# Optimization experiments

Measured on AMD Instinct MI355X. Metric: run time of the kernel, lower is better.

## Reference

```python
import jax, jax.numpy as jnp
import numpy as np

N = 50000; E = 200000; H = 128; L = 3; T = 2; FOUT = 64
G = 1000; NP = 3; ATOM_V = 64; BOND_V = 8
EPS = 1e-5
_DEG_HIST = np.array([0., 50000., 75000., 50000., 25000.])
# PyG PNAConv: avg_deg['log'] = sum(hist[d] * log(d+1)) / num_nodes
AVG_DEG_LOG = float((np.log(np.arange(5) + 1.0) * _DEG_HIST).sum() / _DEG_HIST.sum())


def _bn(v, g, b):
    # training-mode BatchNorm1d (biased variance), eps=1e-5
    mu = v.mean(0)
    var = ((v - mu) ** 2).mean(0)
    return (v - mu) * jax.lax.rsqrt(var + EPS) * g + b


def setup_inputs() -> dict:
    key = jax.random.key(0)
    ks = jax.random.split(key, 16)
    def nrm(k, shape, fan):
        return (jax.random.normal(k, shape, dtype=jnp.float32) / np.sqrt(fan)).astype(jnp.float32)
    return {
        'x': jax.random.randint(ks[0], (N, 9), 0, ATOM_V),
        'edge_index': jax.random.randint(ks[1], (2, E), 0, N),
        'batch': jnp.sort(jax.random.randint(ks[2], (N,), 0, G)),
        'edge_attr_idx': jax.random.randint(ks[3], (E, 3), 0, BOND_V),
        'atom_emb': nrm(ks[4], (9, ATOM_V, H), H),
        'bond_emb': nrm(ks[5], (3, BOND_V, H), H),
        'edge_W': nrm(ks[6], (L, H, H), H), 'edge_b': jnp.zeros((L, H), jnp.float32),
        'pre_W': nrm(ks[7], (L, T, 3 * H, H), 3 * H), 'pre_b': jnp.zeros((L, T, H), jnp.float32),
        'post_W': nrm(ks[8], (L, T, 13 * H, FOUT), 13 * H), 'post_b': jnp.zeros((L, T, FOUT), jnp.float32),
        'lin_W': nrm(ks[9], (L, H, H), H), 'lin_b': jnp.zeros((L, H), jnp.float32),
        'bn_g': jnp.ones((L, H), jnp.float32), 'bn_b': jnp.zeros((L, H), jnp.float32),
        'mlp_W': nrm(ks[10], (2, H, H), H), 'mlp_b': jnp.zeros((2, H), jnp.float32),
        'mlp_g': jnp.ones((2, H), jnp.float32), 'mlp_be': jnp.zeros((2, H), jnp.float32),
        'hW1': nrm(ks[11], (H, H // 2), H), 'hb1': jnp.zeros((H // 2,), jnp.float32),
        'hg1': jnp.ones((H // 2,), jnp.float32), 'hbe1': jnp.zeros((H // 2,), jnp.float32),
        'hW2': nrm(ks[12], (H // 2, H // 4), H // 2), 'hb2': jnp.zeros((H // 4,), jnp.float32),
        'hg2': jnp.ones((H // 4,), jnp.float32), 'hbe2': jnp.zeros((H // 4,), jnp.float32),
        'hW3': nrm(ks[13], (H // 4, NP), H // 4), 'hb3': jnp.zeros((NP,), jnp.float32),
    }


def reference(x, edge_index, batch, edge_attr_idx, atom_emb, bond_emb,
              edge_W, edge_b, pre_W, pre_b, post_W, post_b, lin_W, lin_b,
              bn_g, bn_b, mlp_W, mlp_b, mlp_g, mlp_be,
              hW1, hb1, hg1, hbe1, hW2, hb2, hg2, hbe2, hW3, hb3):
    # encoders: sum of per-feature embeddings (OGB Atom/Bond encoder)
    h = atom_emb[jnp.arange(9), x].sum(1)               # [N,H]
    e = bond_emb[jnp.arange(3), edge_attr_idx].sum(1)   # [E,H]
    src, dst = edge_index[0], edge_index[1]
    cnt = jax.ops.segment_sum(jnp.ones((E,), jnp.float32), dst, N)
    deg = jnp.maximum(cnt, 1.0)[:, None, None]          # clamp(1), as in PyG scalers
    amp = jnp.log(deg + 1.0) / AVG_DEG_LOG
    att = AVG_DEG_LOG / jnp.log(deg + 1.0)
    has = (cnt > 0)[:, None, None]
    for l in range(L):
        ea = e @ edge_W[l] + edge_b[l]                                  # [E,H]
        msg_in = jnp.concatenate([h[dst], h[src], ea], -1)              # [E,3H]
        m = jnp.einsum('ef,tfh->eth', msg_in, pre_W[l]) + pre_b[l]      # [E,T,H]
        s1 = jax.ops.segment_sum(m, dst, N)
        s2 = jax.ops.segment_sum(m * m, dst, N)
        mean = s1 / deg
        std = jnp.sqrt(jax.nn.relu(s2 / deg - mean * mean) + EPS)
        mn = jnp.where(has, jax.ops.segment_min(m, dst, N), 0.0)
        mx = jnp.where(has, jax.ops.segment_max(m, dst, N), 0.0)
        agg = jnp.concatenate([mean, mn, mx, std], -1)                  # [N,T,4H]
        scaled = jnp.concatenate([agg, agg * amp, agg * att], -1)       # [N,T,12H]
        upd = jnp.concatenate(
            [jnp.broadcast_to(h[:, None, :], (N, T, H)), scaled], -1)   # [N,T,13H]
        o = jnp.einsum('ntf,tfo->nto', upd, post_W[l]) + post_b[l]      # [N,T,FOUT]
        o = o.reshape(N, T * FOUT) @ lin_W[l] + lin_b[l]                # [N,H]
        h = jax.nn.relu(_bn(o, bn_g[l], bn_b[l]))
    g = jax.ops.segment_sum(h, batch, G)                                # [G,H]
    for i in range(2):
        g = jax.nn.relu(_bn(g @ mlp_W[i] + mlp_b[i], mlp_g[i], mlp_be[i]))
    g = jax.nn.relu(_bn(g @ hW1 + hb1, hg1, hbe1))
    g = jax.nn.relu(_bn(g @ hW2 + hb2, hg2, hbe2))
    return g @ hW3 + hb3                                                # [G,NP]
```

## Files before the change

kernel.cpp:

```cpp
#include <hip/hip_runtime.h>
#include <math.h>


#define NN 50000
#define NE 200000
#define HD 128
#define NG 1000
#define EPSV 1e-5f
#define ALOGC 1.1330197327247628f

#define AP 1288
#define OPF 132
#define ECAP 512
#define SCB 49

typedef __bf16 bf16x8 __attribute__((ext_vector_type(8)));
typedef float f32x4 __attribute__((ext_vector_type(4)));

__device__ __forceinline__ unsigned short f2bf(float f) {
    unsigned int u = __float_as_uint(f);
    unsigned int r = (u + 0x7FFFu + ((u >> 16) & 1u)) >> 16;
    return (unsigned short)r;
}
__device__ __forceinline__ float bf2f(unsigned short h) {
    return __uint_as_float((unsigned int)h << 16);
}

__global__ void k_fill(float* __restrict__ o, float v, int n) {
    int i = blockIdx.x * 256 + threadIdx.x;
    if (i < n) o[i] = v;
}

__global__ void k_zero(float* __restrict__ z, int n) {
    int i = blockIdx.x * 256 + threadIdx.x;
    if (i < n) z[i] = 0.f;
}

__global__ __launch_bounds__(256) void k_encode_nodes(
    const int* __restrict__ x, const float* __restrict__ aemb, float* __restrict__ h) {
    __shared__ int xi[8][9];
    int nb = blockIdx.x * 8;
    int tid = threadIdx.x;
    if (tid < 72) xi[tid / 9][tid % 9] = x[nb * 9 + tid];
    __syncthreads();
    int node = tid >> 5, c4 = (tid & 31) * 4;
    float4 acc = make_float4(0.f, 0.f, 0.f, 0.f);
#pragma unroll
    for (int f = 0; f < 9; ++f) {
        float4 e = *(const float4*)(aemb + (size_t)(f * 64 + xi[node][f]) * HD + c4);
        acc.x += e.x; acc.y += e.y; acc.z += e.z; acc.w += e.w;
    }
    *(float4*)(h + (size_t)(nb + node) * HD + c4) = acc;
}

__global__ void k_count(const int* __restrict__ dst, int* __restrict__ cnt) {
    int e = blockIdx.x * 256 + threadIdx.x;
    if (e < NE) atomicAdd(&cnt[dst[e]], 1);
}

__global__ __launch_bounds__(1024) void k_scanA(const int* __restrict__ cnt,
                                                int* __restrict__ sc, int* __restrict__ tot) {
    __shared__ int buf[1024];
    int tid = threadIdx.x;
    int i = blockIdx.x * 1024 + tid;
    int v = (i < NN) ? cnt[i] : 0;
    buf[tid] = v;
    __syncthreads();
    for (int s = 1; s < 1024; s <<= 1) {
        int t = (tid >= s) ? buf[tid - s] : 0;
        __syncthreads();
        buf[tid] += t;
        __syncthreads();
    }
    if (i < NN) sc[i] = buf[tid];
    if (tid == 1023) tot[blockIdx.x] = buf[1023];
}

__global__ void k_scanB(const int* __restrict__ tot, int* __restrict__ offb) {
    if (threadIdx.x == 0) {
        int run = 0;
        for (int b = 0; b < SCB; ++b) { offb[b] = run; run += tot[b]; }
    }
}

__global__ __launch_bounds__(1024) void k_scanC(
    const int* __restrict__ cnt, const int* __restrict__ sc, const int* __restrict__ offb,
    int* __restrict__ rowptr, float* __restrict__ ampv, float* __restrict__ attv) {
    int i = blockIdx.x * 1024 + threadIdx.x;
    if (i == 0) rowptr[0] = 0;
    if (i < NN) {
        rowptr[i + 1] = offb[blockIdx.x] + sc[i];
        int v = cnt[i];
        float dg = (float)(v > 0 ? v : 1);
        float lg = logf(dg + 1.0f);
        ampv[i] = lg / ALOGC;
        attv[i] = ALOGC / lg;
    }
}

__global__ void k_scatter(const int* __restrict__ ei, const int* __restrict__ eai,
                          const int* __restrict__ rowptr,
                          int* __restrict__ fill, int* __restrict__ precs) {
    int e = blockIdx.x * 256 + threadIdx.x;
    if (e < NE) {
        int d = ei[NE + e];
        int pos = rowptr[d] + atomicAdd(&fill[d], 1);
        int cidx = eai[e * 3] | (eai[e * 3 + 1] << 3) | (eai[e * 3 + 2] << 6);
        precs[pos] = ei[e] | (cidx << 17);
    }
}

__global__ void k_fold(const float* __restrict__ edge_W, const float* __restrict__ edge_b,
                       const float* __restrict__ pre_W, const float* __restrict__ pre_b,
                       float* __restrict__ cW, float* __restrict__ tb) {
    int l = blockIdx.y;
    int k = blockIdx.x;
    int tj = threadIdx.x;
    int t = tj >> 7, j = tj & 127;
    const float* pw = pre_W + ((size_t)(l * 2 + t) * 384 + 256) * 128 + j;
    if (k < 128) {
        const float* ew = edge_W + ((size_t)l * 128 + k) * 128;
        float acc = 0.f;
        for (int i = 0; i < 128; ++i) acc += ew[i] * pw[i * 128];
        cW[((size_t)l * 128 + k) * 256 + tj] = acc;
    } else {
        const float* eb = edge_b + l * 128;
        float acc = pre_b[(l * 2 + t) * 128 + j];
        for (int i = 0; i < 128; ++i) acc += eb[i] * pw[i * 128];
        tb[l * 256 + tj] = acc;
    }
}

__global__ void k_bcomb2(const float* __restrict__ bemb, const float* __restrict__ cW,
                         unsigned short* __restrict__ bcomb) {
    int ci = blockIdx.x, l = blockIdx.y, tj = threadIdx.x;
    const float* s0 = bemb + (size_t)(0 * 8 + (ci & 7)) * 128;
    const float* s1 = bemb + (size_t)(1 * 8 + ((ci >> 3) & 7)) * 128;
    const float* s2 = bemb + (size_t)(2 * 8 + (ci >> 6)) * 128;
    const float* w = cW + (size_t)l * 128 * 256;
    float acc = 0.f;
    for (int i = 0; i < 128; ++i) acc += (s0[i] + s1[i] + s2[i]) * w[i * 256 + tj];
    bcomb[((size_t)l * 512 + ci) * 256 + tj] = f2bf(acc);
}

__device__ __forceinline__ void pack_body2(const float* __restrict__ W, int N, int NT,
                                           unsigned short* __restrict__ pkh,
                                           unsigned short* __restrict__ pkl,
                                           int blk, int lane) {
    int kstep = blk / NT, nt = blk - kstep * NT;
    int kb = kstep * 32 + (lane >> 4) * 8;
    int col = nt * 16 + (lane & 15);
    unsigned short th[8], tl[8];
#pragma unroll
    for (int i = 0; i < 8; ++i) {
        float w = W[(size_t)(kb + i) * N + col];
        unsigned short hh = f2bf(w);
        th[i] = hh;
        tl[i] = f2bf(w - bf2f(hh));
    }
    size_t base = ((size_t)blk * 64 + lane) * 8;
    *(uint4*)(pkh + base) = *(uint4*)th;
    *(uint4*)(pkl + base) = *(uint4*)tl;
}

__global__ __launch_bounds__(64) void k_packall(
    const float* __restrict__ post_W, const float* __restrict__ lin_W,
    const float* __restrict__ pre_W,
    unsigned short* __restrict__ pkPostHi, unsigned short* __restrict__ pkPostLo,
    unsigned short* __restrict__ pkLinHi, unsigned short* __restrict__ pkLinLo,
    unsigned short* __restrict__ pkPreHi, unsigned short* __restrict__ pkPreLo) {
    int b = blockIdx.x;
    int lane = threadIdx.x;
    if (b < 1248) {
        int l = b / 416, rem = b % 416;
        int t = rem / 208, blk = rem % 208;
        size_t off = ((size_t)l * 2 + t) * 106496;
        pack_body2(post_W + ((size_t)l * 2 + t) * 1664 * 64, 64, 4,
                   pkPostHi + off, pkPostLo + off, blk, lane);
    } else if (b < 1344) {
        int idx = b - 1248;
        int l = idx / 32, blk = idx % 32;
        pack_body2(lin_W + (size_t)l * 128 * 128, 128, 8,
                   pkLinHi + (size_t)l * 16384, pkLinLo + (size_t)l * 16384, blk, lane);
    } else {
        int idx = b - 1344;
        int l = idx / 128, bb = idx % 128;
        const float* preW = pre_W + (size_t)l * 2 * 384 * 128;
        unsigned short* phi = pkPreHi + (size_t)l * 65536;
        unsigned short* plo = pkPreLo + (size_t)l * 65536;
        int kstep = bb >> 5, nt = bb & 31;
        int q = lane >> 4, nc = lane & 15;
        int col = nt * 16 + nc;
        int t = (col >> 7) & 1;
        int jcol = col & 127;
        int fbase = (col < 256) ? 0 : 128;
        unsigned short hi[8], lo[8];
#pragma unroll
        for (int i = 0; i < 8; ++i) {
            int k = kstep * 32 + q * 8 + i;
            float w = preW[((size_t)t * 384 + fbase + k) * 128 + jcol];
            unsigned short h16 = f2bf(w);
            hi[i] = h16;
            lo[i] = f2bf(w - bf2f(h16));
        }
        size_t base = ((size_t)bb * 64 + lane) * 8;
        *(uint4*)(phi + base) = *(uint4*)hi;
        *(uint4*)(plo + base) = *(uint4*)lo;
    }
}

__device__ __forceinline__ void pre_mfma_body2(
    const unsigned short* __restrict__ ah, const unsigned short* __restrict__ al,
    const unsigned short* __restrict__ phi, const unsigned short* __restrict__ plo,
    const float* __restrict__ tb, int n0, int tid,
    unsigned short* __restrict__ hzd, unsigned short* __restrict__ hzs) {
    int lane = tid & 63, w = tid >> 6;
    int q = lane >> 4, nc = lane & 15;
    f32x4 acc0[8], acc1[8];
#pragma unroll
    for (int j = 0; j < 8; ++j) {
        acc0[j] = (f32x4){0.f, 0.f, 0.f, 0.f};
        acc1[j] = (f32x4){0.f, 0.f, 0.f, 0.f};
    }
#pragma unroll
    for (int kk = 0; kk < 4; ++kk) {
        bf16x8 Ahi0 = *(const bf16x8*)(ah + nc * 136 + kk * 32 + q * 8);
        bf16x8 Alo0 = *(const bf16x8*)(al + nc * 136 + kk * 32 + q * 8);
        bf16x8 Ahi1 = *(const bf16x8*)(ah + (16 + nc) * 136 + kk * 32 + q * 8);
        bf16x8 Alo1 = *(const bf16x8*)(al + (16 + nc) * 136 + kk * 32 + q * 8);
#pragma unroll
        for (int j = 0; j < 8; ++j) {
            int nt = w * 8 + j;
            size_t base = ((size_t)(kk * 32 + nt) * 64 + lane) * 8;
            bf16x8 Bhi = *(const bf16x8*)(phi + base);
            bf16x8 Blo = *(const bf16x8*)(plo + base);
            acc0[j] = __builtin_amdgcn_mfma_f32_16x16x32_bf16(Ahi0, Bhi, acc0[j], 0, 0, 0);
            acc0[j] = __builtin_amdgcn_mfma_f32_16x16x32_bf16(Ahi0, Blo, acc0[j], 0, 0, 0);
            acc0[j] = __builtin_amdgcn_mfma_f32_16x16x32_bf16(Alo0, Bhi, acc0[j], 0, 0, 0);
            acc1[j] = __builtin_amdgcn_mfma_f32_16x16x32_bf16(Ahi1, Bhi, acc1[j], 0, 0, 0);
            acc1[j] = __builtin_amdgcn_mfma_f32_16x16x32_bf16(Ahi1, Blo, acc1[j], 0, 0, 0);
            acc1[j] = __builtin_amdgcn_mfma_f32_16x16x32_bf16(Alo1, Bhi, acc1[j], 0, 0, 0);
        }
    }
#pragma unroll
    for (int j = 0; j < 8; ++j) {
        int col = (w * 8 + j) * 16 + nc;
        float bias = (col < 256) ? tb[col] : 0.f;
#pragma unroll
        for (int reg = 0; reg < 4; ++reg) {
            int r0 = n0 + q * 4 + reg;
            int r1 = r0 + 16;
            if (col < 256) {
                if (r0 < NN) hzd[(size_t)r0 * 256 + col] = f2bf(acc0[j][reg] + bias);
                if (r1 < NN) hzd[(size_t)r1 * 256 + col] = f2bf(acc1[j][reg] + bias);
            } else {
                if (r0 < NN) hzs[(size_t)r0 * 256 + (col - 256)] = f2bf(acc0[j][reg]);
                if (r1 < NN) hzs[(size_t)r1 * 256 + (col - 256)] = f2bf(acc1[j][reg]);
            }
        }
    }
}

__global__ __launch_bounds__(256) void k_pre_m(
    const float* __restrict__ h,
    const unsigned short* __restrict__ phi, const unsigned short* __restrict__ plo,
    const float* __restrict__ tb,
    unsigned short* __restrict__ hzd, unsigned short* __restrict__ hzs) {
    __shared__ __align__(16) unsigned short ah[32 * 136];
    __shared__ __align__(16) unsigned short al[32 * 136];
    int n0 = blockIdx.x * 32;
    int tid = threadIdx.x;
    for (int half = 0; half < 2; ++half) {
        int node = (tid >> 4) + half * 16, cg = (tid & 15) * 8;
        int n = n0 + node;
        unsigned short hh[8] = {0, 0, 0, 0, 0, 0, 0, 0};
        unsigned short ll[8] = {0, 0, 0, 0, 0, 0, 0, 0};
        if (n < NN) {
            const float* hs = h + (size_t)n * HD + cg;
            float4 v0 = *(const float4*)(hs);
            float4 v1 = *(const float4*)(hs + 4);
            float vv[8] = {v0.x, v0.y, v0.z, v0.w, v1.x, v1.y, v1.z, v1.w};
#pragma unroll
            for (int i = 0; i < 8; ++i) {
                hh[i] = f2bf(vv[i]);
                ll[i] = f2bf(vv[i] - bf2f(hh[i]));
            }
        }
        *(uint4*)(ah + node * 136 + cg) = *(uint4*)hh;
        *(uint4*)(al + node * 136 + cg) = *(uint4*)ll;
    }
    __syncthreads();
    pre_mfma_body2(ah, al, phi, plo, tb, n0, tid, hzd, hzs);
}

__global__ __launch_bounds__(256) void k_bnpre(
    const float* __restrict__ o2, const float* __restrict__ stats,
    const float* __restrict__ g, const float* __restrict__ b,
    const unsigned short* __restrict__ phi, const unsigned short* __restrict__ plo,
    const float* __restrict__ tb,
    float* __restrict__ h, unsigned short* __restrict__ hzd, unsigned short* __restrict__ hzs) {
    __shared__ __align__(16) unsigned short ah[32 * 136];
    __shared__ __align__(16) unsigned short al[32 * 136];
    int n0 = blockIdx.x * 32;
    int tid = threadIdx.x;
    for (int half = 0; half < 2; ++half) {
        int node = (tid >> 4) + half * 16, cg = (tid & 15) * 8;
        int n = n0 + node;
        unsigned short hh[8] = {0, 0, 0, 0, 0, 0, 0, 0};
        unsigned short ll[8] = {0, 0, 0, 0, 0, 0, 0, 0};
        if (n < NN) {
            const float* os = o2 + (size_t)n * HD + cg;
            float4 v0 = *(const float4*)(os);
            float4 v1 = *(const float4*)(os + 4);
            float vv[8] = {v0.x, v0.y, v0.z, v0.w, v1.x, v1.y, v1.z, v1.w};
            float ou[8];
#pragma unroll
            for (int i = 0; i < 8; ++i) {
                int c = cg + i;
                float mu = stats[c] * (1.f / NN);
                float var = stats[128 + c] * (1.f / NN) - mu * mu;
                float val = (vv[i] - mu) * rsqrtf(var + EPSV) * g[c] + b[c];
                val = fmaxf(val, 0.f);
                ou[i] = val;
                hh[i] = f2bf(val);
                ll[i] = f2bf(val - bf2f(hh[i]));
            }
            float* hd = h + (size_t)n * HD + cg;
            *(float4*)(hd) = make_float4(ou[0], ou[1], ou[2], ou[3]);
            *(float4*)(hd + 4) = make_float4(ou[4], ou[5], ou[6], ou[7]);
        }
        *(uint4*)(ah + node * 136 + cg) = *(uint4*)hh;
        *(uint4*)(al + node * 136 + cg) = *(uint4*)ll;
    }
    __syncthreads();
    pre_mfma_body2(ah, al, phi, plo, tb, n0, tid, hzd, hzs);
}

__global__ __launch_bounds__(256) void k_post(
    const float* __restrict__ h,
    const unsigned short* __restrict__ hzd, const unsigned short* __restrict__ hzs,
    const int* __restrict__ rowptr, const int* __restrict__ precs,
    const unsigned short* __restrict__ bcomb,
    const float* __restrict__ ampv, const float* __restrict__ attv,
    const unsigned short* __restrict__ pkPostHi, const unsigned short* __restrict__ pkPostLo,
    const float* __restrict__ postb,
    const unsigned short* __restrict__ pkLinHi, const unsigned short* __restrict__ pkLinLo,
    const float* __restrict__ linb,
    float* __restrict__ o2, float* __restrict__ stats) {
    __shared__ __align__(16) unsigned short a_lds[16 * AP];
    __shared__ __align__(16) float o_f[16 * OPF];
    __shared__ int es[ECAP];
    __shared__ float s_amp[16], s_att[16];
    int n0 = blockIdx.x * 16;
    int tid = threadIdx.x;

    int pbase = rowptr[n0];
    int ecount = rowptr[n0 + 16] - pbase;
    for (int i = tid; i < ecount && i < ECAP; i += 256) es[i] = precs[pbase + i];
    {
        int node = tid >> 4, cg = (tid & 15) * 8;
        const float* hs = h + (size_t)(n0 + node) * HD + cg;
        float4 v0 = *(const float4*)(hs);
        float4 v1 = *(const float4*)(hs + 4);
        unsigned short* d0 = a_lds + node * AP + cg;
        unsigned short* d1 = d0 + 640;
        unsigned short bb[8];
        bb[0] = f2bf(v0.x); bb[1] = f2bf(v0.y); bb[2] = f2bf(v0.z); bb[3] = f2bf(v0.w);
        bb[4] = f2bf(v1.x); bb[5] = f2bf(v1.y); bb[6] = f2bf(v1.z); bb[7] = f2bf(v1.w);
#pragma unroll
        for (int i = 0; i < 8; ++i) { d0[i] = bb[i]; d1[i] = bb[i]; }
    }
    if (tid < 16) { s_amp[tid] = ampv[n0 + tid]; s_att[tid] = attv[n0 + tid]; }
    __syncthreads();

    {
        int wv = tid >> 6, lane = tid & 63;
        int cc = lane * 4;
        int tt = cc >> 7, jj = cc & 127;
        bool incap = (ecount <= ECAP);
        const float4 Z4 = make_float4(0.f, 0.f, 0.f, 0.f);
        const float4 BIG = make_float4(3.4e38f, 3.4e38f, 3.4e38f, 3.4e38f);
        const float4 NBIG = make_float4(-3.4e38f, -3.4e38f, -3.4e38f, -3.4e38f);

#define EDGE_ACC(P, S1, S2, MN, MX)                                                       \
        {                                                                                 \
            int rec = incap ? es[(P) - pbase] : precs[(P)];                               \
            int sp = rec & 131071;                                                        \
            int ci = rec >> 17;                                                           \
            uint2 uv = *(const uint2*)(hzs + (size_t)sp * 256 + cc);                      \
            uint2 ub = *(const uint2*)(bcomb + (size_t)ci * 256 + cc);                    \
            float wx = __uint_as_float(uv.x << 16) + __uint_as_float(ub.x << 16);         \
            float wy = __uint_as_float(uv.x & 0xffff0000u) + __uint_as_float(ub.x & 0xffff0000u); \
            float wz = __uint_as_float(uv.y << 16) + __uint_as_float(ub.y << 16);         \
            float ww = __uint_as_float(uv.y & 0xffff0000u) + __uint_as_float(ub.y & 0xffff0000u); \
            S1.x += wx; S1.y += wy; S1.z += wz; S1.w += ww;                               \
            S2.x += wx * wx; S2.y += wy * wy; S2.z += wz * wz; S2.w += ww * ww;           \
            MN.x = fminf(MN.x, wx); MN.y = fminf(MN.y, wy);                               \
            MN.z = fminf(MN.z, wz); MN.w = fminf(MN.w, ww);                               \
            MX.x = fmaxf(MX.x, wx); MX.y = fmaxf(MX.y, wy);                               \
            MX.z = fmaxf(MX.z, wz); MX.w = fmaxf(MX.w, ww);                               \
        }

        auto fin = [&](int r, int cnt, float4 hd, float4 s1, float4 s2, float4 mn, float4 mx) {
            float inv = 1.f / (float)(cnt > 0 ? cnt : 1);
            float4 mw, stdv, mean;
            mw.x = s1.x * inv; mw.y = s1.y * inv; mw.z = s1.z * inv; mw.w = s1.w * inv;
            stdv.x = sqrtf(fmaxf(s2.x * inv - mw.x * mw.x, 0.f) + EPSV);
            stdv.y = sqrtf(fmaxf(s2.y * inv - mw.y * mw.y, 0.f) + EPSV);
            stdv.z = sqrtf(fmaxf(s2.z * inv - mw.z * mw.z, 0.f) + EPSV);
            stdv.w = sqrtf(fmaxf(s2.w * inv - mw.w * mw.w, 0.f) + EPSV);
            if (cnt > 0) {
                mean.x = hd.x + mw.x; mean.y = hd.y + mw.y;
                mean.z = hd.z + mw.z; mean.w = hd.w + mw.w;
                mn.x += hd.x; mn.y += hd.y; mn.z += hd.z; mn.w += hd.w;
                mx.x += hd.x; mx.y += hd.y; mx.z += hd.z; mx.w += hd.w;
            } else {
                mean = Z4; mn = Z4; mx = Z4;
            }
            unsigned short* d = a_lds + r * AP + tt * 640 + 128 + jj;
            d[0] = f2bf(mean.x); d[1] = f2bf(mean.y); d[2] = f2bf(mean.z); d[3] = f2bf(mean.w);
            d += 128; d[0] = f2bf(mn.x); d[1] = f2bf(mn.y); d[2] = f2bf(mn.z); d[3] = f2bf(mn.w);
            d += 128; d[0] = f2bf(mx.x); d[1] = f2bf(mx.y); d[2] = f2bf(mx.z); d[3] = f2bf(mx.w);
            d += 128; d[0] = f2bf(stdv.x); d[1] = f2bf(stdv.y); d[2] = f2bf(stdv.z); d[3] = f2bf(stdv.w);
        };

        for (int i = 0; i < 2; ++i) {
            int ra = wv * 4 + i * 2;
            int rb = ra + 1;
            int na = n0 + ra, nb = n0 + rb;
            int pa0 = rowptr[na], pa1 = rowptr[na + 1];
            int pb0 = rowptr[nb], pb1 = rowptr[nb + 1];
            uint2 uda = *(const uint2*)(hzd + (size_t)na * 256 + cc);
            uint2 udb = *(const uint2*)(hzd + (size_t)nb * 256 + cc);
            float4 hda, hdb;
            hda.x = __uint_as_float(uda.x << 16); hda.y = __uint_as_float(uda.x & 0xffff0000u);
            hda.z = __uint_as_float(uda.y << 16); hda.w = __uint_as_float(uda.y & 0xffff0000u);
            hdb.x = __uint_as_float(udb.x << 16); hdb.y = __uint_as_float(udb.x & 0xffff0000u);
            hdb.z = __uint_as_float(udb.y << 16); hdb.w = __uint_as_float(udb.y & 0xffff0000u);
            float4 s1a = Z4, s2a = Z4, mna = BIG, mxa = NBIG;
            float4 s1b = Z4, s2b = Z4, mnb = BIG, mxb = NBIG;
            int da = pa1 - pa0, db = pb1 - pb0;
            int mc = (da < db) ? da : db;
            for (int k = 0; k < mc; ++k) {
                EDGE_ACC(pa0 + k, s1a, s2a, mna, mxa)
                EDGE_ACC(pb0 + k, s1b, s2b, mnb, mxb)
            }
            for (int k = mc; k < da; ++k) EDGE_ACC(pa0 + k, s1a, s2a, mna, mxa)
            for (int k = mc; k < db; ++k) EDGE_ACC(pb0 + k, s1b, s2b, mnb, mxb)
            fin(ra, da, hda, s1a, s2a, mna, mxa);
            fin(rb, db, hdb, s1b, s2b, mnb, mxb);
        }
#undef EDGE_ACC
    }
    __syncthreads();

    {
        int lane = tid & 63;
        int w = tid >> 6;
        int t = w >> 1;
        int ntb = (w & 1) * 2;
        int q = lane >> 4, nc = lane & 15;
        const unsigned short* arow = a_lds + (size_t)nc * AP + t * 640 + q * 8;
        size_t toff = (size_t)t * 106496;
        const unsigned short* pkh = pkPostHi + toff;
        const unsigned short* pkl = pkPostLo + toff;
        f32x4 aP0 = {0.f, 0.f, 0.f, 0.f}, aP1 = {0.f, 0.f, 0.f, 0.f};
        f32x4 aA0 = {0.f, 0.f, 0.f, 0.f}, aA1 = {0.f, 0.f, 0.f, 0.f};
        f32x4 aT0 = {0.f, 0.f, 0.f, 0.f}, aT1 = {0.f, 0.f, 0.f, 0.f};
        for (int kk = 0; kk < 20; ++kk) {
            bf16x8 af = *(const bf16x8*)(arow + kk * 32);
            size_t ib = ((size_t)(kk * 4 + ntb) * 64 + lane) * 8;
            aP0 = __builtin_amdgcn_mfma_f32_16x16x32_bf16(af, *(const bf16x8*)(pkh + ib), aP0, 0, 0, 0);
            aP0 = __builtin_amdgcn_mfma_f32_16x16x32_bf16(af, *(const bf16x8*)(pkl + ib), aP0, 0, 0, 0);
            aP1 = __builtin_amdgcn_mfma_f32_16x16x32_bf16(af, *(const bf16x8*)(pkh + ib + 512), aP1, 0, 0, 0);
            aP1 = __builtin_amdgcn_mfma_f32_16x16x32_bf16(af, *(const bf16x8*)(pkl + ib + 512), aP1, 0, 0, 0);
            if (kk >= 4) {
                size_t ia = ((size_t)((kk + 16) * 4 + ntb) * 64 + lane) * 8;
                aA0 = __builtin_amdgcn_mfma_f32_16x16x32_bf16(af, *(const bf16x8*)(pkh + ia), aA0, 0, 0, 0);
                aA0 = __builtin_amdgcn_mfma_f32_16x16x32_bf16(af, *(const bf16x8*)(pkl + ia), aA0, 0, 0, 0);
                aA1 = __builtin_amdgcn_mfma_f32_16x16x32_bf16(af, *(const bf16x8*)(pkh + ia + 512), aA1, 0, 0, 0);
                aA1 = __builtin_amdgcn_mfma_f32_16x16x32_bf16(af, *(const bf16x8*)(pkl + ia + 512), aA1, 0, 0, 0);
                size_t it = ((size_t)((kk + 32) * 4 + ntb) * 64 + lane) * 8;
                aT0 = __builtin_amdgcn_mfma_f32_16x16x32_bf16(af, *(const bf16x8*)(pkh + it), aT0, 0, 0, 0);
                aT0 = __builtin_amdgcn_mfma_f32_16x16x32_bf16(af, *(const bf16x8*)(pkl + it), aT0, 0, 0, 0);
                aT1 = __builtin_amdgcn_mfma_f32_16x16x32_bf16(af, *(const bf16x8*)(pkh + it + 512), aT1, 0, 0, 0);
                aT1 = __builtin_amdgcn_mfma_f32_16x16x32_bf16(af, *(const bf16x8*)(pkl + it + 512), aT1, 0, 0, 0);
            }
        }
#pragma unroll
        for (int u = 0; u < 2; ++u) {
            int nt = ntb + u;
            int col = t * 64 + nt * 16 + nc;
            float pbia = postb[t * 64 + nt * 16 + nc];
            f32x4 P = u ? aP1 : aP0;
            f32x4 A = u ? aA1 : aA0;
            f32x4 T = u ? aT1 : aT0;
#pragma unroll
            for (int reg = 0; reg < 4; ++reg) {
                int mrow = q * 4 + reg;
                o_f[mrow * OPF + col] = P[reg] + s_amp[mrow] * A[reg] + s_att[mrow] * T[reg] + pbia;
            }
        }
    }
    __syncthreads();

    {
        int lane = tid & 63;
        int w = tid >> 6;
        int ntb = w * 2;
        int q = lane >> 4, nc = lane & 15;
        const float* arow = o_f + (size_t)nc * OPF + q * 8;
        f32x4 L0 = {0.f, 0.f, 0.f, 0.f}, L1 = {0.f, 0.f, 0.f, 0.f};
#pragma unroll
        for (int kk = 0; kk < 4; ++kk) {
            float4 a0 = *(const float4*)(arow + kk * 32);
            float4 a1 = *(const float4*)(arow + kk * 32 + 4);
            float vv[8] = {a0.x, a0.y, a0.z, a0.w, a1.x, a1.y, a1.z, a1.w};
            unsigned short hh[8], ll[8];
#pragma unroll
            for (int i = 0; i < 8; ++i) {
                hh[i] = f2bf(vv[i]);
                ll[i] = f2bf(vv[i] - bf2f(hh[i]));
            }
            bf16x8 Ahi = *(const bf16x8*)hh;
            bf16x8 Alo = *(const bf16x8*)ll;
            size_t ib = ((size_t)(kk * 8 + ntb) * 64 + lane) * 8;
            bf16x8 B0h = *(const bf16x8*)(pkLinHi + ib);
            bf16x8 B0l = *(const bf16x8*)(pkLinLo + ib);
            bf16x8 B1h = *(const bf16x8*)(pkLinHi + ib + 512);
            bf16x8 B1l = *(const bf16x8*)(pkLinLo + ib + 512);
            L0 = __builtin_amdgcn_mfma_f32_16x16x32_bf16(Ahi, B0h, L0, 0, 0, 0);
            L0 = __builtin_amdgcn_mfma_f32_16x16x32_bf16(Alo, B0h, L0, 0, 0, 0);
            L0 = __builtin_amdgcn_mfma_f32_16x16x32_bf16(Ahi, B0l, L0, 0, 0, 0);
            L1 = __builtin_amdgcn_mfma_f32_16x16x32_bf16(Ahi, B1h, L1, 0, 0, 0);
            L1 = __builtin_amdgcn_mfma_f32_16x16x32_bf16(Alo, B1h, L1, 0, 0, 0);
            L1 = __builtin_amdgcn_mfma_f32_16x16x32_bf16(Ahi, B1l, L1, 0, 0, 0);
        }
#pragma unroll
        for (int u = 0; u < 2; ++u) {
            int col = (ntb + u) * 16 + nc;
            float lb = linb[col];
            f32x4 L = u ? L1 : L0;
            float ps = 0.f, pss = 0.f;
#pragma unroll
            for (int reg = 0; reg < 4; ++reg) {
                int mrow = q * 4 + reg;
                float v = L[reg] + lb;
                o2[(size_t)(n0 + mrow) * HD + col] = v;
                ps += v; pss += v * v;
            }
            ps += __shfl_down(ps, 16); ps += __shfl_down(ps, 32);
            pss += __shfl_down(pss, 16); pss += __shfl_down(pss, 32);
            if (q == 0) {
                atomicAdd(&stats[col], ps);
                atomicAdd(&stats[128 + col], pss);
            }
        }
    }
}

__global__ void k_pool(const float* __restrict__ o2, const float* __restrict__ stats,
                       const float* __restrict__ g, const float* __restrict__ b,
                       const int* __restrict__ batch, float* __restrict__ g0) {
    int c = threadIdx.x;
    float mu = stats[c] * (1.f / NN);
    float var = stats[128 + c] * (1.f / NN) - mu * mu;
    float rs = rsqrtf(var + EPSV) * g[c];
    float bb = b[c];
    int nbase = blockIdx.x * 64;
    float run = 0.f; int cur = -1;
    for (int i = 0; i < 64; ++i) {
        int n = nbase + i;
        if (n >= NN) break;
        int bi = batch[n];
        if (bi != cur) {
            if (cur >= 0) atomicAdd(&g0[(size_t)cur * HD + c], run);
            cur = bi; run = 0.f;
        }
        run += fmaxf((o2[(size_t)n * HD + c] - mu) * rs + bb, 0.f);
    }
    if (cur >= 0) atomicAdd(&g0[(size_t)cur * HD + c], run);
}

__global__ void k_head_gemm(const float* __restrict__ x, const float* __restrict__ W,
                            const float* __restrict__ b, float* __restrict__ y,
                            float* __restrict__ stats, int K, int Kout) {
    int row = blockIdx.x;
    int col = threadIdx.x;
    if (col >= Kout) return;
    float acc = b[col];
    for (int k = 0; k < K; k += 4) {
        float4 xv = *(const float4*)(x + (size_t)row * K + k);
        acc += xv.x * W[(k + 0) * Kout + col] + xv.y * W[(k + 1) * Kout + col]
             + xv.z * W[(k + 2) * Kout + col] + xv.w * W[(k + 3) * Kout + col];
    }
    y[(size_t)row * Kout + col] = acc;
    if (stats) {
        atomicAdd(&stats[col], acc);
        atomicAdd(&stats[Kout + col], acc * acc);
    }
}

__global__ __launch_bounds__(128) void k_head_fused(
    const float* __restrict__ y_in, const float* __restrict__ stats_in,
    const float* __restrict__ g, const float* __restrict__ b,
    const float* __restrict__ W, const float* __restrict__ bias,
    float* __restrict__ y_out, float* __restrict__ stats_out, int Kin, int Kout) {
    __shared__ float row[128];
    int r = blockIdx.x, tid = threadIdx.x;
    if (tid < Kin) {
        float mu = stats_in[tid] * (1.f / NG);
        float var = stats_in[Kin + tid] * (1.f / NG) - mu * mu;
        float v = (y_in[(size_t)r * Kin + tid] - mu) * rsqrtf(var + EPSV) * g[tid] + b[tid];
        row[tid] = fmaxf(v, 0.f);
    }
    __syncthreads();
    if (tid < Kout) {
        float acc = bias[tid];
        for (int k = 0; k < Kin; ++k) acc += row[k] * W[(size_t)k * Kout + tid];
        y_out[(size_t)r * Kout + tid] = acc;
        if (stats_out) {
            atomicAdd(&stats_out[tid], acc);
            atomicAdd(&stats_out[Kout + tid], acc * acc);
        }
    }
}

extern "C" void kernel_launch(void* const* d_in, const int* in_sizes, int n_in,
                              void* d_out, int out_size, void* d_ws, size_t ws_size,
                              hipStream_t stream) {
    const int*   x        = (const int*)  d_in[0];
    const int*   ei       = (const int*)  d_in[1];
    const int*   batch    = (const int*)  d_in[2];
    const int*   eai      = (const int*)  d_in[3];
    const float* atom_emb = (const float*)d_in[4];
    const float* bond_emb = (const float*)d_in[5];
    const float* edge_W   = (const float*)d_in[6];
    const float* edge_b   = (const float*)d_in[7];
    const float* pre_W    = (const float*)d_in[8];
    const float* pre_b    = (const float*)d_in[9];
    const float* post_W   = (const float*)d_in[10];
    const float* post_b   = (const float*)d_in[11];
    const float* lin_W    = (const float*)d_in[12];
    const float* lin_b    = (const float*)d_in[13];
    const float* bn_g     = (const float*)d_in[14];
    const float* bn_b     = (const float*)d_in[15];
    const float* mlp_W    = (const float*)d_in[16];
    const float* mlp_b    = (const float*)d_in[17];
    const float* mlp_g    = (const float*)d_in[18];
    const float* mlp_be   = (const float*)d_in[19];
    const float* hW1 = (const float*)d_in[20]; const float* hb1  = (const float*)d_in[21];
    const float* hg1 = (const float*)d_in[22]; const float* hbe1 = (const float*)d_in[23];
    const float* hW2 = (const float*)d_in[24]; const float* hb2  = (const float*)d_in[25];
    const float* hg2 = (const float*)d_in[26]; const float* hbe2 = (const float*)d_in[27];
    const float* hW3 = (const float*)d_in[28]; const float* hb3  = (const float*)d_in[29];
    float* out = (float*)d_out;
    (void)n_in; (void)in_sizes;

    char* p = (char*)d_ws;
    size_t off = 0;
    auto alloc = [&](size_t bytes) -> char* {
        char* r = p + off;
        off += (bytes + 255) & ~(size_t)255;
        return r;
    };
    float* h     = (float*)alloc((size_t)NN * HD * 4);
    float* o2    = (float*)alloc((size_t)NN * HD * 4);
    unsigned short* hzd = (unsigned short*)alloc((size_t)NN * 256 * 2);
    unsigned short* hzs = (unsigned short*)alloc((size_t)NN * 256 * 2);
    float* ampv  = (float*)alloc((size_t)NN * 4);
    float* attv  = (float*)alloc((size_t)NN * 4);
    int*   rowptr= (int*)  alloc((size_t)(NN + 1) * 4);
    int*   precs = (int*)  alloc((size_t)NE * 4);
    int*   sc    = (int*)  alloc((size_t)NN * 4);
    int*   stot  = (int*)  alloc((size_t)SCB * 4);
    int*   soff  = (int*)  alloc((size_t)SCB * 4);
    float* cW    = (float*)alloc((size_t)3 * 128 * 256 * 4);
    float* tbb   = (float*)alloc((size_t)3 * 256 * 4);
    unsigned short* bcomb = (unsigned short*)alloc((size_t)3 * 512 * 256 * 2);
    unsigned short* pkPostHi = (unsigned short*)alloc((size_t)3 * 2 * 106496 * 2);
    unsigned short* pkPostLo = (unsigned short*)alloc((size_t)3 * 2 * 106496 * 2);
    unsigned short* pkLinHi  = (unsigned short*)alloc((size_t)3 * 16384 * 2);
    unsigned short* pkLinLo  = (unsigned short*)alloc((size_t)3 * 16384 * 2);
    unsigned short* pkPreHi  = (unsigned short*)alloc((size_t)3 * 65536 * 2);
    unsigned short* pkPreLo  = (unsigned short*)alloc((size_t)3 * 65536 * 2);
    float* gA    = (float*)alloc((size_t)NG * HD * 4);
    float* gB    = (float*)alloc((size_t)NG * HD * 4);
    char* z0 = p + off;
    int*   cnt   = (int*)  alloc((size_t)NN * 4);
    int*   fill  = (int*)  alloc((size_t)NN * 4);
    float* stats = (float*)alloc((size_t)3 * 256 * 4);
    float* hstats= (float*)alloc((size_t)4 * 256 * 4);
    float* g0    = (float*)alloc((size_t)NG * HD * 4);
    size_t zwords = (size_t)((p + off) - z0) / 4;

    if (off > ws_size) {
        k_fill<<<(out_size + 255) / 256, 256, 0, stream>>>(out, (float)ws_size, out_size);
        return;
    }

    k_zero<<<(int)((zwords + 255) / 256), 256, 0, stream>>>((float*)z0, (int)zwords);
    k_encode_nodes<<<NN / 8, 256, 0, stream>>>(x, atom_emb, h);
    k_count<<<(NE + 255) / 256, 256, 0, stream>>>(ei + NE, cnt);
    k_scanA<<<SCB, 1024, 0, stream>>>(cnt, sc, stot);
    k_scanB<<<1, 64, 0, stream>>>(stot, soff);
    k_scanC<<<SCB, 1024, 0, stream>>>(cnt, sc, soff, rowptr, ampv, attv);
    k_scatter<<<(NE + 255) / 256, 256, 0, stream>>>(ei, eai, rowptr, fill, precs);
    k_fold<<<dim3(129, 3), 256, 0, stream>>>(edge_W, edge_b, pre_W, pre_b, cW, tbb);
    k_bcomb2<<<dim3(512, 3), 256, 0, stream>>>(bond_emb, cW, bcomb);
    k_packall<<<1728, 64, 0, stream>>>(post_W, lin_W, pre_W,
        pkPostHi, pkPostLo, pkLinHi, pkLinLo, pkPreHi, pkPreLo);

    int preBlocks = (NN + 31) / 32;
    for (int l = 0; l < 3; ++l) {
        if (l == 0) {
            k_pre_m<<<preBlocks, 256, 0, stream>>>(h, pkPreHi, pkPreLo, tbb, hzd, hzs);
        } else {
            k_bnpre<<<preBlocks, 256, 0, stream>>>(o2, stats + (l - 1) * 256,
                bn_g + (l - 1) * 128, bn_b + (l - 1) * 128,
                pkPreHi + (size_t)l * 65536, pkPreLo + (size_t)l * 65536,
                tbb + l * 256, h, hzd, hzs);
        }
        k_post<<<NN / 16, 256, 0, stream>>>(h, hzd, hzs, rowptr, precs,
            bcomb + (size_t)l * 512 * 256,
            ampv, attv,
            pkPostHi + (size_t)l * 2 * 106496, pkPostLo + (size_t)l * 2 * 106496,
            post_b + l * 2 * 64,
            pkLinHi + (size_t)l * 16384, pkLinLo + (size_t)l * 16384,
            lin_b + l * 128,
            o2, stats + l * 256);
    }

    k_pool<<<(NN + 63) / 64, 128, 0, stream>>>(o2, stats + 2 * 256,
        bn_g + 2 * 128, bn_b + 2 * 128, batch, g0);

    k_head_gemm<<<NG, 128, 0, stream>>>(g0, mlp_W, mlp_b, gA, hstats, 128, 128);
    k_head_fused<<<NG, 128, 0, stream>>>(gA, hstats, mlp_g, mlp_be,
        mlp_W + 128 * 128, mlp_b + 128, gB, hstats + 256, 128, 128);
    k_head_fused<<<NG, 128, 0, stream>>>(gB, hstats + 256, mlp_g + 128, mlp_be + 128,
        hW1, hb1, gA, hstats + 512, 128, 64);
    k_head_fused<<<NG, 128, 0, stream>>>(gA, hstats + 512, hg1, hbe1,
        hW2, hb2, gB, hstats + 768, 64, 32);
    k_head_fused<<<NG, 128, 0, stream>>>(gB, hstats + 768, hg2, hbe2,
        hW3, hb3, out, (float*)nullptr, 32, 3);
}
```

Measured before the change: 924.9 us.

## Process 32 nodes per k_post block so each weight fragment serves two row tiles

```diff
diff --git a/kernel.cpp b/kernel.cpp
--- a/kernel.cpp
+++ b/kernel.cpp
@@ -11,7 +11,7 @@
 
 #define AP 1288
 #define OPF 132
-#define ECAP 512
+#define ECAP2 1024
 #define SCB 49
 
 typedef __bf16 bf16x8 __attribute__((ext_vector_type(8)));
@@ -336,7 +336,7 @@
     pre_mfma_body2(ah, al, phi, plo, tb, n0, tid, hzd, hzs);
 }
 
-__global__ __launch_bounds__(256) void k_post(
+__global__ __launch_bounds__(512) void k_post(
     const float* __restrict__ h,
     const unsigned short* __restrict__ hzd, const unsigned short* __restrict__ hzs,
     const int* __restrict__ rowptr, const int* __restrict__ precs,
@@ -347,37 +347,45 @@
     const unsigned short* __restrict__ pkLinHi, const unsigned short* __restrict__ pkLinLo,
     const float* __restrict__ linb,
     float* __restrict__ o2, float* __restrict__ stats) {
-    __shared__ __align__(16) unsigned short a_lds[16 * AP];
-    __shared__ __align__(16) float o_f[16 * OPF];
-    __shared__ int es[ECAP];
-    __shared__ float s_amp[16], s_att[16];
-    int n0 = blockIdx.x * 16;
+    __shared__ __align__(16) unsigned short a_lds[32 * AP];
+    __shared__ __align__(16) float o_f[32 * OPF];
+    __shared__ int es[ECAP2];
+    __shared__ float s_amp[32], s_att[32];
+    int n0 = blockIdx.x * 32;
     int tid = threadIdx.x;
+    int nEnd = (n0 + 32 < NN) ? (n0 + 32) : NN;
 
     int pbase = rowptr[n0];
-    int ecount = rowptr[n0 + 16] - pbase;
-    for (int i = tid; i < ecount && i < ECAP; i += 256) es[i] = precs[pbase + i];
+    int ecount = rowptr[nEnd] - pbase;
+    for (int i = tid; i < ecount && i < ECAP2; i += 512) es[i] = precs[pbase + i];
     {
         int node = tid >> 4, cg = (tid & 15) * 8;
-        const float* hs = h + (size_t)(n0 + node) * HD + cg;
-        float4 v0 = *(const float4*)(hs);
-        float4 v1 = *(const float4*)(hs + 4);
+        int n = n0 + node;
+        unsigned short bb[8] = {0, 0, 0, 0, 0, 0, 0, 0};
+        if (n < NN) {
+            const float* hs = h + (size_t)n * HD + cg;
+            float4 v0 = *(const float4*)(hs);
+            float4 v1 = *(const float4*)(hs + 4);
+            bb[0] = f2bf(v0.x); bb[1] = f2bf(v0.y); bb[2] = f2bf(v0.z); bb[3] = f2bf(v0.w);
+            bb[4] = f2bf(v1.x); bb[5] = f2bf(v1.y); bb[6] = f2bf(v1.z); bb[7] = f2bf(v1.w);
+        }
         unsigned short* d0 = a_lds + node * AP + cg;
         unsigned short* d1 = d0 + 640;
-        unsigned short bb[8];
-        bb[0] = f2bf(v0.x); bb[1] = f2bf(v0.y); bb[2] = f2bf(v0.z); bb[3] = f2bf(v0.w);
-        bb[4] = f2bf(v1.x); bb[5] = f2bf(v1.y); bb[6] = f2bf(v1.z); bb[7] = f2bf(v1.w);
 #pragma unroll
         for (int i = 0; i < 8; ++i) { d0[i] = bb[i]; d1[i] = bb[i]; }
     }
-    if (tid < 16) { s_amp[tid] = ampv[n0 + tid]; s_att[tid] = attv[n0 + tid]; }
+    if (tid < 32) {
+        int n = n0 + tid;
+        s_amp[tid] = (n < NN) ? ampv[n] : 1.f;
+        s_att[tid] = (n < NN) ? attv[n] : 1.f;
+    }
     __syncthreads();
 
     {
         int wv = tid >> 6, lane = tid & 63;
         int cc = lane * 4;
         int tt = cc >> 7, jj = cc & 127;
-        bool incap = (ecount <= ECAP);
+        bool incap = (ecount <= ECAP2);
         const float4 Z4 = make_float4(0.f, 0.f, 0.f, 0.f);
         const float4 BIG = make_float4(3.4e38f, 3.4e38f, 3.4e38f, 3.4e38f);
         const float4 NBIG = make_float4(-3.4e38f, -3.4e38f, -3.4e38f, -3.4e38f);
@@ -428,15 +436,20 @@
             int ra = wv * 4 + i * 2;
             int rb = ra + 1;
             int na = n0 + ra, nb = n0 + rb;
-            int pa0 = rowptr[na], pa1 = rowptr[na + 1];
-            int pb0 = rowptr[nb], pb1 = rowptr[nb + 1];
-            uint2 uda = *(const uint2*)(hzd + (size_t)na * 256 + cc);
-            uint2 udb = *(const uint2*)(hzd + (size_t)nb * 256 + cc);
-            float4 hda, hdb;
-            hda.x = __uint_as_float(uda.x << 16); hda.y = __uint_as_float(uda.x & 0xffff0000u);
-            hda.z = __uint_as_float(uda.y << 16); hda.w = __uint_as_float(uda.y & 0xffff0000u);
-            hdb.x = __uint_as_float(udb.x << 16); hdb.y = __uint_as_float(udb.x & 0xffff0000u);
-            hdb.z = __uint_as_float(udb.y << 16); hdb.w = __uint_as_float(udb.y & 0xffff0000u);
+            int pa0 = 0, pa1 = 0, pb0 = 0, pb1 = 0;
+            float4 hda = Z4, hdb = Z4;
+            if (na < NN) {
+                pa0 = rowptr[na]; pa1 = rowptr[na + 1];
+                uint2 uda = *(const uint2*)(hzd + (size_t)na * 256 + cc);
+                hda.x = __uint_as_float(uda.x << 16); hda.y = __uint_as_float(uda.x & 0xffff0000u);
+                hda.z = __uint_as_float(uda.y << 16); hda.w = __uint_as_float(uda.y & 0xffff0000u);
+            }
+            if (nb < NN) {
+                pb0 = rowptr[nb]; pb1 = rowptr[nb + 1];
+                uint2 udb = *(const uint2*)(hzd + (size_t)nb * 256 + cc);
+                hdb.x = __uint_as_float(udb.x << 16); hdb.y = __uint_as_float(udb.x & 0xffff0000u);
+                hdb.z = __uint_as_float(udb.y << 16); hdb.w = __uint_as_float(udb.y & 0xffff0000u);
+            }
             float4 s1a = Z4, s2a = Z4, mna = BIG, mxa = NBIG;
             float4 s1b = Z4, s2b = Z4, mnb = BIG, mxb = NBIG;
             int da = pa1 - pa0, db = pb1 - pb0;
@@ -457,48 +470,55 @@
     {
         int lane = tid & 63;
         int w = tid >> 6;
-        int t = w >> 1;
-        int ntb = (w & 1) * 2;
+        int t = w >> 2;
+        int ntIn = w & 3;
         int q = lane >> 4, nc = lane & 15;
-        const unsigned short* arow = a_lds + (size_t)nc * AP + t * 640 + q * 8;
+        const unsigned short* arow0 = a_lds + (size_t)nc * AP + t * 640 + q * 8;
+        const unsigned short* arow1 = a_lds + (size_t)(16 + nc) * AP + t * 640 + q * 8;
         size_t toff = (size_t)t * 106496;
         const unsigned short* pkh = pkPostHi + toff;
         const unsigned short* pkl = pkPostLo + toff;
-        f32x4 aP0 = {0.f, 0.f, 0.f, 0.f}, aP1 = {0.f, 0.f, 0.f, 0.f};
-        f32x4 aA0 = {0.f, 0.f, 0.f, 0.f}, aA1 = {0.f, 0.f, 0.f, 0.f};
-        f32x4 aT0 = {0.f, 0.f, 0.f, 0.f}, aT1 = {0.f, 0.f, 0.f, 0.f};
+        f32x4 P0 = {0.f, 0.f, 0.f, 0.f}, P1 = {0.f, 0.f, 0.f, 0.f};
+        f32x4 A0 = {0.f, 0.f, 0.f, 0.f}, A1 = {0.f, 0.f, 0.f, 0.f};
+        f32x4 T0 = {0.f, 0.f, 0.f, 0.f}, T1 = {0.f, 0.f, 0.f, 0.f};
         for (int kk = 0; kk < 20; ++kk) {
-            bf16x8 af = *(const bf16x8*)(arow + kk * 32);
-            size_t ib = ((size_t)(kk * 4 + ntb) * 64 + lane) * 8;
-            aP0 = __builtin_amdgcn_mfma_f32_16x16x32_bf16(af, *(const bf16x8*)(pkh + ib), aP0, 0, 0, 0);
-            aP0 = __builtin_amdgcn_mfma_f32_16x16x32_bf16(af, *(const bf16x8*)(pkl + ib), aP0, 0, 0, 0);
-            aP1 = __builtin_amdgcn_mfma_f32_16x16x32_bf16(af, *(const bf16x8*)(pkh + ib + 512), aP1, 0, 0, 0);
-            aP1 = __builtin_amdgcn_mfma_f32_16x16x32_bf16(af, *(const bf16x8*)(pkl + ib + 512), aP1, 0, 0, 0);
+            bf16x8 af0 = *(const bf16x8*)(arow0 + kk * 32);
+            bf16x8 af1 = *(const bf16x8*)(arow1 + kk * 32);
+            size_t ib = ((size_t)(kk * 4 + ntIn) * 64 + lane) * 8;
+            bf16x8 Bh = *(const bf16x8*)(pkh + ib);
+            bf16x8 Bl = *(const bf16x8*)(pkl + ib);
+            P0 = __builtin_amdgcn_mfma_f32_16x16x32_bf16(af0, Bh, P0, 0, 0, 0);
+            P0 = __builtin_amdgcn_mfma_f32_16x16x32_bf16(af0, Bl, P0, 0, 0, 0);
+            P1 = __builtin_amdgcn_mfma_f32_16x16x32_bf16(af1, Bh, P1, 0, 0, 0);
+            P1 = __builtin_amdgcn_mfma_f32_16x16x32_bf16(af1, Bl, P1, 0, 0, 0);
             if (kk >= 4) {
-                size_t ia = ((size_t)((kk + 16) * 4 + ntb) * 64 + lane) * 8;
-                aA0 = __builtin_amdgcn_mfma_f32_16x16x32_bf16(af, *(const bf16x8*)(pkh + ia), aA0, 0, 0, 0);
-                aA0 = __builtin_amdgcn_mfma_f32_16x16x32_bf16(af, *(const bf16x8*)(pkl + ia), aA0, 0, 0, 0);
-                aA1 = __builtin_amdgcn_mfma_f32_16x16x32_bf16(af, *(const bf16x8*)(pkh + ia + 512), aA1, 0, 0, 0);
-                aA1 = __builtin_amdgcn_mfma_f32_16x16x32_bf16(af, *(const bf16x8*)(pkl + ia + 512), aA1, 0, 0, 0);
-                size_t it = ((size_t)((kk + 32) * 4 + ntb) * 64 + lane) * 8;
-                aT0 = __builtin_amdgcn_mfma_f32_16x16x32_bf16(af, *(const bf16x8*)(pkh + it), aT0, 0, 0, 0);
-                aT0 = __builtin_amdgcn_mfma_f32_16x16x32_bf16(af, *(const bf16x8*)(pkl + it), aT0, 0, 0, 0);
-                aT1 = __builtin_amdgcn_mfma_f32_16x16x32_bf16(af, *(const bf16x8*)(pkh + it + 512), aT1, 0, 0, 0);
-                aT1 = __builtin_amdgcn_mfma_f32_16x16x32_bf16(af, *(const bf16x8*)(pkl + it + 512), aT1, 0, 0, 0);
-            }
-        }
-#pragma unroll
-        for (int u = 0; u < 2; ++u) {
-            int nt = ntb + u;
-            int col = t * 64 + nt * 16 + nc;
-            float pbia = postb[t * 64 + nt * 16 + nc];
-            f32x4 P = u ? aP1 : aP0;
-            f32x4 A = u ? aA1 : aA0;
-            f32x4 T = u ? aT1 : aT0;
+                size_t ia = ((size_t)((kk + 16) * 4 + ntIn) * 64 + lane) * 8;
+                bf16x8 Ah = *(const bf16x8*)(pkh + ia);
+                bf16x8 Al = *(const bf16x8*)(pkl + ia);
+                A0 = __builtin_amdgcn_mfma_f32_16x16x32_bf16(af0, Ah, A0, 0, 0, 0);
+                A0 = __builtin_amdgcn_mfma_f32_16x16x32_bf16(af0, Al, A0, 0, 0, 0);
+                A1 = __builtin_amdgcn_mfma_f32_16x16x32_bf16(af1, Ah, A1, 0, 0, 0);
+                A1 = __builtin_amdgcn_mfma_f32_16x16x32_bf16(af1, Al, A1, 0, 0, 0);
+                size_t it = ((size_t)((kk + 32) * 4 + ntIn) * 64 + lane) * 8;
+                bf16x8 Th = *(const bf16x8*)(pkh + it);
+                bf16x8 Tl = *(const bf16x8*)(pkl + it);
+                T0 = __builtin_amdgcn_mfma_f32_16x16x32_bf16(af0, Th, T0, 0, 0, 0);
+                T0 = __builtin_amdgcn_mfma_f32_16x16x32_bf16(af0, Tl, T0, 0, 0, 0);
+                T1 = __builtin_amdgcn_mfma_f32_16x16x32_bf16(af1, Th, T1, 0, 0, 0);
+                T1 = __builtin_amdgcn_mfma_f32_16x16x32_bf16(af1, Tl, T1, 0, 0, 0);
+            }
+        }
+        int col = t * 64 + ntIn * 16 + nc;
+        float pbia = postb[col];
+#pragma unroll
+        for (int m = 0; m < 2; ++m) {
+            f32x4 P = m ? P1 : P0;
+            f32x4 A = m ? A1 : A0;
+            f32x4 T = m ? T1 : T0;
 #pragma unroll
             for (int reg = 0; reg < 4; ++reg) {
-                int mrow = q * 4 + reg;
-                o_f[mrow * OPF + col] = P[reg] + s_amp[mrow] * A[reg] + s_att[mrow] * T[reg] + pbia;
+                int row = m * 16 + q * 4 + reg;
+                o_f[row * OPF + col] = P[reg] + s_amp[row] * A[reg] + s_att[row] * T[reg] + pbia;
             }
         }
     }
@@ -507,54 +527,60 @@
     {
         int lane = tid & 63;
         int w = tid >> 6;
-        int ntb = w * 2;
         int q = lane >> 4, nc = lane & 15;
-        const float* arow = o_f + (size_t)nc * OPF + q * 8;
+        const float* arow0 = o_f + (size_t)nc * OPF + q * 8;
+        const float* arow1 = o_f + (size_t)(16 + nc) * OPF + q * 8;
         f32x4 L0 = {0.f, 0.f, 0.f, 0.f}, L1 = {0.f, 0.f, 0.f, 0.f};
 #pragma unroll
         for (int kk = 0; kk < 4; ++kk) {
-            float4 a0 = *(const float4*)(arow + kk * 32);
-            float4 a1 = *(const float4*)(arow + kk * 32 + 4);
-            float vv[8] = {a0.x, a0.y, a0.z, a0.w, a1.x, a1.y, a1.z, a1.w};
-            unsigned short hh[8], ll[8];
+            float4 a0 = *(const float4*)(arow0 + kk * 32);
+            float4 a1 = *(const float4*)(arow0 + kk * 32 + 4);
+            float4 b0 = *(const float4*)(arow1 + kk * 32);
+            float4 b1 = *(const float4*)(arow1 + kk * 32 + 4);
+            float v0[8] = {a0.x, a0.y, a0.z, a0.w, a1.x, a1.y, a1.z, a1.w};
+            float v1[8] = {b0.x, b0.y, b0.z, b0.w, b1.x, b1.y, b1.z, b1.w};
+            unsigned short h0[8], l0[8], h1[8], l1[8];
 #pragma unroll
             for (int i = 0; i < 8; ++i) {
-                hh[i] = f2bf(vv[i]);
-                ll[i] = f2bf(vv[i] - bf2f(hh[i]));
-            }
-            bf16x8 Ahi = *(const bf16x8*)hh;
-            bf16x8 Alo = *(const bf16x8*)ll;
-            size_t ib = ((size_t)(kk * 8 + ntb) * 64 + lane) * 8;
-            bf16x8 B0h = *(const bf16x8*)(pkLinHi + ib);
-            bf16x8 B0l = *(const bf16x8*)(pkLinLo + ib);
-            bf16x8 B1h = *(const bf16x8*)(pkLinHi + ib + 512);
-            bf16x8 B1l = *(const bf16x8*)(pkLinLo + ib + 512);
-            L0 = __builtin_amdgcn_mfma_f32_16x16x32_bf16(Ahi, B0h, L0, 0, 0, 0);
-            L0 = __builtin_amdgcn_mfma_f32_16x16x32_bf16(Alo, B0h, L0, 0, 0, 0);
-            L0 = __builtin_amdgcn_mfma_f32_16x16x32_bf16(Ahi, B0l, L0, 0, 0, 0);
-            L1 = __builtin_amdgcn_mfma_f32_16x16x32_bf16(Ahi, B1h, L1, 0, 0, 0);
-            L1 = __builtin_amdgcn_mfma_f32_16x16x32_bf16(Alo, B1h, L1, 0, 0, 0);
-            L1 = __builtin_amdgcn_mfma_f32_16x16x32_bf16(Ahi, B1l, L1, 0, 0, 0);
-        }
-#pragma unroll
-        for (int u = 0; u < 2; ++u) {
-            int col = (ntb + u) * 16 + nc;
-            float lb = linb[col];
-            f32x4 L = u ? L1 : L0;
-            float ps = 0.f, pss = 0.f;
+                h0[i] = f2bf(v0[i]); l0[i] = f2bf(v0[i] - bf2f(h0[i]));
+                h1[i] = f2bf(v1[i]); l1[i] = f2bf(v1[i] - bf2f(h1[i]));
+            }
+            bf16x8 Ahi0 = *(const bf16x8*)h0;
+            bf16x8 Alo0 = *(const bf16x8*)l0;
+            bf16x8 Ahi1 = *(const bf16x8*)h1;
+            bf16x8 Alo1 = *(const bf16x8*)l1;
+            size_t ib = ((size_t)(kk * 8 + w) * 64 + lane) * 8;
+            bf16x8 Bh = *(const bf16x8*)(pkLinHi + ib);
+            bf16x8 Bl = *(const bf16x8*)(pkLinLo + ib);
+            L0 = __builtin_amdgcn_mfma_f32_16x16x32_bf16(Ahi0, Bh, L0, 0, 0, 0);
+            L0 = __builtin_amdgcn_mfma_f32_16x16x32_bf16(Alo0, Bh, L0, 0, 0, 0);
+            L0 = __builtin_amdgcn_mfma_f32_16x16x32_bf16(Ahi0, Bl, L0, 0, 0, 0);
+            L1 = __builtin_amdgcn_mfma_f32_16x16x32_bf16(Ahi1, Bh, L1, 0, 0, 0);
+            L1 = __builtin_amdgcn_mfma_f32_16x16x32_bf16(Alo1, Bh, L1, 0, 0, 0);
+            L1 = __builtin_amdgcn_mfma_f32_16x16x32_bf16(Ahi1, Bl, L1, 0, 0, 0);
+        }
+        int col = w * 16 + nc;
+        float lb = linb[col];
+        float ps = 0.f, pss = 0.f;
+#pragma unroll
+        for (int m = 0; m < 2; ++m) {
+            f32x4 L = m ? L1 : L0;
 #pragma unroll
             for (int reg = 0; reg < 4; ++reg) {
-                int mrow = q * 4 + reg;
+                int row = m * 16 + q * 4 + reg;
+                int gn = n0 + row;
                 float v = L[reg] + lb;
-                o2[(size_t)(n0 + mrow) * HD + col] = v;
-                ps += v; pss += v * v;
-            }
-            ps += __shfl_down(ps, 16); ps += __shfl_down(ps, 32);
-            pss += __shfl_down(pss, 16); pss += __shfl_down(pss, 32);
-            if (q == 0) {
-                atomicAdd(&stats[col], ps);
-                atomicAdd(&stats[128 + col], pss);
-            }
+                if (gn < NN) {
+                    o2[(size_t)gn * HD + col] = v;
+                    ps += v; pss += v * v;
+                }
+            }
+        }
+        ps += __shfl_down(ps, 16); ps += __shfl_down(ps, 32);
+        pss += __shfl_down(pss, 16); pss += __shfl_down(pss, 32);
+        if (q == 0) {
+            atomicAdd(&stats[col], ps);
+            atomicAdd(&stats[128 + col], pss);
         }
     }
 }
@@ -721,7 +747,7 @@
                 pkPreHi + (size_t)l * 65536, pkPreLo + (size_t)l * 65536,
                 tbb + l * 256, h, hzd, hzs);
         }
-        k_post<<<NN / 16, 256, 0, stream>>>(h, hzd, hzs, rowptr, precs,
+        k_post<<<preBlocks, 512, 0, stream>>>(h, hzd, hzs, rowptr, precs,
             bcomb + (size_t)l * 512 * 256,
             ampv, attv,
             pkPostHi + (size_t)l * 2 * 106496, pkPostLo + (size_t)l * 2 * 106496,
```

New measurement: 1.139 ms. 23.2% more time.
